# Optimization experiments

Hardware: AMD Instinct MI355X
Metric: run time of the kernel (lower is better)

The kernel has to match this reference:

```python
import jax, jax.numpy as jnp
import numpy as np

# Static graph layout: B graphs, NPG nodes/graph, CNUM com edges, MPG BatchReversal rows/graph
B, NPG, CNUM, MPG = 512, 64, 8, 128
CN, CE, HN, HE = 256, 64, 4, 4          # node channels, edge channels, heads
EPG = MPG + CNUM + NPG                   # edge_inform rows (= edges) per graph = 200


def _seg_softmax(logits, seg, num):
    # softmax over segments (per-destination) along axis 0; logits [E, H]
    m = jax.ops.segment_max(logits, seg, num_segments=num)
    m = jnp.where(jnp.isfinite(m), m, 0.0)
    e = jnp.exp(logits - m[seg])
    s = jax.ops.segment_sum(e, seg, num_segments=num)
    return e / (s[seg] + 1e-16)


def _attn_conv(x, edge_index, Wq, Wk, Wv, heads, e=None, We=None):
    # Multi-head edge-conditioned graph attention (SuperConv_N / SuperConv_E).
    N = x.shape[0]
    O = Wq.shape[1]
    Oh = O // heads
    q = (x @ Wq).reshape(N, heads, Oh)
    k = (x @ Wk).reshape(N, heads, Oh)
    v = (x @ Wv).reshape(N, heads, Oh)
    src, dst = edge_index[0], edge_index[1]
    ks, vs = k[src], v[src]
    if e is not None:
        ef = (e @ We).reshape(-1, heads, Oh)
        ks = ks + ef
        vs = vs + ef
    scale = jnp.asarray(1.0 / np.sqrt(Oh), x.dtype)
    logits = jax.nn.leaky_relu(jnp.sum(q[dst] * ks, axis=-1) * scale, 0.2)  # [E, H]
    alpha = _seg_softmax(logits, dst, N)
    out = jax.ops.segment_sum(alpha[..., None] * vs, dst, num_segments=N)  # [N, H, Oh]
    return out.reshape(N, O)


def _bn(x, g, b):
    # pyg_nn.BatchNorm, training mode: batch statistics over node axis
    mu = x.mean(axis=0)
    var = x.var(axis=0)
    return (x - mu) * jax.lax.rsqrt(var + 1e-5) * g + b


def _to_edge(br):
    # Vectorized BatchReversalToEdge: per graph, first CNUM rows duplicated
    # consecutively, then NPG one-hot rows, then the remaining MPG-CNUM rows.
    sub = br.reshape(B, MPG, CE)
    dup = jnp.repeat(sub[:, :CNUM], 2, axis=1)                     # [B, 2c, CE]
    onehot = jnp.zeros((CE,), br.dtype).at[0].set(1.0)
    blk = jnp.broadcast_to(onehot, (B, NPG, CE))                   # [B, n, CE]
    out = jnp.concatenate([dup, blk, sub[:, CNUM:]], axis=1)       # [B, EPG, CE]
    return out.reshape(B * EPG, CE)


def setup_inputs() -> dict:
    key = jax.random.key(0)
    ks = jax.random.split(key, 20)
    Nn = B * NPG
    x = jax.random.normal(ks[0], (Nn, CN), jnp.float32)
    base_n = jnp.repeat(jnp.arange(B) * NPG, EPG)
    edge_index = base_n[None, :] + jax.random.randint(ks[1], (2, B * EPG), 0, NPG)
    br_feature = jax.random.normal(ks[2], (B * MPG, CE), jnp.float32)
    base_e = jnp.repeat(jnp.arange(B) * MPG, MPG * 4)
    br_edge_index = base_e[None, :] + jax.random.randint(ks[3], (2, B * MPG * 4), 0, MPG)

    def w(k, i, o):
        return jax.random.normal(k, (i, o), jnp.float32) / np.sqrt(i)

    inp = dict(x=x, edge_index=edge_index, br_feature=br_feature, br_edge_index=br_edge_index)
    inp.update(WqE1=w(ks[4], CE, CE), WkE1=w(ks[5], CE, CE), WvE1=w(ks[6], CE, CE),
               gE1=jnp.ones(CE), bE1=jnp.zeros(CE))
    inp.update(Wq1=w(ks[7], CN, CN), Wk1=w(ks[8], CN, CN), Wv1=w(ks[9], CN, CN),
               We1=w(ks[10], CE, CN), gN1=jnp.ones(CN), bN1=jnp.zeros(CN))
    inp.update(WqE2=w(ks[11], CE, CE), WkE2=w(ks[12], CE, CE), WvE2=w(ks[13], CE, CE),
               gE2=jnp.ones(CE), bE2=jnp.zeros(CE))
    inp.update(Wq2=w(ks[14], CN, CN), Wk2=w(ks[15], CN, CN), Wv2=w(ks[16], CN, CN),
               We2=w(ks[17], CE, CN), gN2=jnp.ones(CN), bN2=jnp.zeros(CN))
    return inp


def reference(x, edge_index, br_feature, br_edge_index,
              WqE1, WkE1, WvE1, gE1, bE1,
              Wq1, Wk1, Wv1, We1, gN1, bN1,
              WqE2, WkE2, WvE2, gE2, bE2,
              Wq2, Wk2, Wv2, We2, gN2, bN2):
    br = br_feature
    # conv_E -> BN -> ReLU, residual (E_in == E_out)
    o = jax.nn.relu(_bn(_attn_conv(br, br_edge_index, WqE1, WkE1, WvE1, HE), gE1, bE1))
    br = o + br
    ei = _to_edge(br)
    # conv_N -> BN -> ReLU, residual (N_in == N_out)
    o = jax.nn.relu(_bn(_attn_conv(x, edge_index, Wq1, Wk1, Wv1, HN, e=ei, We=We1), gN1, bN1))
    out = o + x
    # conv_E2 -> BN -> ReLU, subtractive residual
    o2 = jax.nn.relu(_bn(_attn_conv(br, br_edge_index, WqE2, WkE2, WvE2, HE), gE2, bE2))
    br = br - o2
    ei = _to_edge(br)
    # conv_N2 -> BN -> ReLU, subtractive residual
    o2 = jax.nn.relu(_bn(_attn_conv(out, edge_index, Wq2, Wk2, Wv2, HN, e=ei, We=We2), gN2, bN2))
    out2 = out - o2
    # GetSuperNode: last node of each graph (regular layout -> simple slice)
    super_node = out2.reshape(B, NPG, CN)[:, -1]
    return out2, ei, br, super_node
```

## Files before the change

kernel.cpp:

```cpp
#include <hip/hip_runtime.h>

typedef unsigned short u16;
typedef unsigned int u32;

#define BGR 512
#define NPG_ 64
#define MPG_ 128
#define EPG_ 200
#define CN_ 256
#define CE_ 64
#define NN_ (BGR*NPG_)
#define NBR_ (BGR*MPG_)
#define EN_ (BGR*EPG_)
#define EBR_ (BGR*MPG_*4)

__device__ __forceinline__ float bf2f(u16 u){ return __uint_as_float(((u32)u) << 16); }
__device__ __forceinline__ u16 f2bf(float f){
  u32 u = __float_as_uint(f);
  u32 r = u + 0x7FFFu + ((u >> 16) & 1u);
  return (u16)(r >> 16);
}
__device__ __forceinline__ void up2(u32 w, float& a, float& b){
  a = bf2f((u16)w); b = bf2f((u16)(w >> 16));
}
__device__ __forceinline__ u32 pk2(u16 a, u16 b){ return (u32)a | ((u32)b << 16); }

typedef __attribute__((ext_vector_type(8))) short short8v;
typedef __attribute__((ext_vector_type(4))) float f32x4;

__global__ __launch_bounds__(256) void zero_k(float* __restrict__ p, size_t n){
  size_t i = (size_t)blockIdx.x*256 + threadIdx.x;
  const size_t st = (size_t)gridDim.x*256;
  for (; i < n; i += st) p[i] = 0.f;
}

template<int BN>
__global__ __launch_bounds__(256) void mfma_gemm2(const float* __restrict__ A,
                                                  const float* __restrict__ W,
                                                  u16* __restrict__ C,
                                                  int M, int N, int K)
{
  constexpr int PK = 40;
  constexpr int NF = (BN == 128) ? 4 : 2;
  constexpr int KPTB = BN / 32;
  __shared__ alignas(16) u16 sAh[128*PK], sAl[128*PK];
  __shared__ alignas(16) u16 sBh[BN*PK],  sBl[BN*PK];

  const int tid = threadIdx.x;
  const int m0 = blockIdx.y * 128, n0 = blockIdx.x * BN;
  const int wid = tid >> 6, lane = tid & 63;
  const int wm = (wid >> 1) * 64;
  const int wn = (wid & 1) * (NF * 16);
  const int l15 = lane & 15, l4 = lane >> 4;
  const int kb = l4 * 8;

  const int arow = tid >> 1, aseg = (tid & 1) * 16;
  const int nq = tid & (BN/4 - 1);
  const int bn = nq * 4;
  const int kq = tid / (BN/4);
  const int bk = kq * KPTB;

  f32x4 acc[4][NF];
  #pragma unroll
  for (int i = 0; i < 4; i++)
    #pragma unroll
    for (int j = 0; j < NF; j++) acc[i][j] = (f32x4)0.f;

  for (int k0 = 0; k0 < K; k0 += 32){
    {
      const float* ap = A + (size_t)(m0 + arow)*K + k0 + aseg;
      u16 hh[16], ll[16];
      #pragma unroll
      for (int j = 0; j < 16; j += 4){
        const float4 av = *(const float4*)(ap + j);
        const float vs0 = av.x, vs1 = av.y, vs2 = av.z, vs3 = av.w;
        u16 h;
        h = f2bf(vs0); hh[j+0] = h; ll[j+0] = f2bf(vs0 - bf2f(h));
        h = f2bf(vs1); hh[j+1] = h; ll[j+1] = f2bf(vs1 - bf2f(h));
        h = f2bf(vs2); hh[j+2] = h; ll[j+2] = f2bf(vs2 - bf2f(h));
        h = f2bf(vs3); hh[j+3] = h; ll[j+3] = f2bf(vs3 - bf2f(h));
      }
      uint4 p;
      p.x = pk2(hh[0],hh[1]);  p.y = pk2(hh[2],hh[3]);
      p.z = pk2(hh[4],hh[5]);  p.w = pk2(hh[6],hh[7]);
      *(uint4*)&sAh[arow*PK + aseg] = p;
      p.x = pk2(hh[8],hh[9]);  p.y = pk2(hh[10],hh[11]);
      p.z = pk2(hh[12],hh[13]); p.w = pk2(hh[14],hh[15]);
      *(uint4*)&sAh[arow*PK + aseg + 8] = p;
      p.x = pk2(ll[0],ll[1]);  p.y = pk2(ll[2],ll[3]);
      p.z = pk2(ll[4],ll[5]);  p.w = pk2(ll[6],ll[7]);
      *(uint4*)&sAl[arow*PK + aseg] = p;
      p.x = pk2(ll[8],ll[9]);  p.y = pk2(ll[10],ll[11]);
      p.z = pk2(ll[12],ll[13]); p.w = pk2(ll[14],ll[15]);
      *(uint4*)&sAl[arow*PK + aseg + 8] = p;
    }
    {
      float bv[KPTB][4];
      #pragma unroll
      for (int j = 0; j < KPTB; j++){
        const float4 w4 = *(const float4*)(W + (size_t)(k0 + bk + j)*N + n0 + bn);
        bv[j][0] = w4.x; bv[j][1] = w4.y; bv[j][2] = w4.z; bv[j][3] = w4.w;
      }
      #pragma unroll
      for (int nn = 0; nn < 4; nn++){
        u16 hh[KPTB], ll[KPTB];
        #pragma unroll
        for (int j = 0; j < KPTB; j++){
          const u16 h = f2bf(bv[j][nn]);
          hh[j] = h; ll[j] = f2bf(bv[j][nn] - bf2f(h));
        }
        if constexpr (KPTB == 4){
          uint2 wr;
          wr.x = pk2(hh[0],hh[1]); wr.y = pk2(hh[2],hh[3]);
          *(uint2*)&sBh[(bn+nn)*PK + bk] = wr;
          wr.x = pk2(ll[0],ll[1]); wr.y = pk2(ll[2],ll[3]);
          *(uint2*)&sBl[(bn+nn)*PK + bk] = wr;
        } else {
          *(u32*)&sBh[(bn+nn)*PK + bk] = pk2(hh[0],hh[1]);
          *(u32*)&sBl[(bn+nn)*PK + bk] = pk2(ll[0],ll[1]);
        }
      }
    }
    __syncthreads();

    short8v ah_[4], al_[4], bh_[NF], bl_[NF];
    #pragma unroll
    for (int mf = 0; mf < 4; mf++){
      ah_[mf] = *(const short8v*)&sAh[(wm + mf*16 + l15)*PK + kb];
      al_[mf] = *(const short8v*)&sAl[(wm + mf*16 + l15)*PK + kb];
    }
    #pragma unroll
    for (int nf = 0; nf < NF; nf++){
      bh_[nf] = *(const short8v*)&sBh[(wn + nf*16 + l15)*PK + kb];
      bl_[nf] = *(const short8v*)&sBl[(wn + nf*16 + l15)*PK + kb];
    }
    #pragma unroll
    for (int nf = 0; nf < NF; nf++)
      #pragma unroll
      for (int mf = 0; mf < 4; mf++){
        acc[mf][nf] = __builtin_amdgcn_mfma_f32_16x16x32_bf16(ah_[mf], bh_[nf], acc[mf][nf], 0, 0, 0);
        acc[mf][nf] = __builtin_amdgcn_mfma_f32_16x16x32_bf16(al_[mf], bh_[nf], acc[mf][nf], 0, 0, 0);
        acc[mf][nf] = __builtin_amdgcn_mfma_f32_16x16x32_bf16(ah_[mf], bl_[nf], acc[mf][nf], 0, 0, 0);
      }
    __syncthreads();
  }

  #pragma unroll
  for (int mf = 0; mf < 4; mf++)
    #pragma unroll
    for (int nf = 0; nf < NF; nf++)
      #pragma unroll
      for (int r = 0; r < 4; r++){
        const int row = m0 + wm + mf*16 + l4*4 + r;
        const int col = n0 + wn + nf*16 + l15;
        C[(size_t)row*N + col] = f2bf(acc[mf][nf][r]);
      }
}

__global__ __launch_bounds__(64) void to_edge_g(const float* __restrict__ br, float* __restrict__ eo)
{
  const int j = blockIdx.x, g = blockIdx.y, c = threadIdx.x;
  float v;
  if (j < 16) v = br[((size_t)g*128 + (j >> 1))*64 + c];
  else if (j < 80) v = (c == 0) ? 1.f : 0.f;
  else v = br[((size_t)g*128 + (j - 72))*64 + c];
  eo[((size_t)g*200 + j)*64 + c] = v;
}

template<int C, int NODES, int EDGES, bool HAS_EF>
__global__ __launch_bounds__(256) void attn_gather(const u16* __restrict__ q,
                                                   const u16* __restrict__ k,
                                                   const u16* __restrict__ v,
                                                   const u16* __restrict__ ef,
                                                   const int* __restrict__ eidx, int Etot,
                                                   float scale,
                                                   float* __restrict__ att)
{
  constexpr int NCH = (EDGES + 63) / 64;
  const int tid = threadIdx.x;
  const int wv = tid >> 6, lane = tid & 63;
  const int d = blockIdx.x*4 + wv;
  const int g = d / NODES;
  const int e0 = g * EDGES;

  float q0, q1, q2, q3;
  if (C == 256){
    const uint2 qa = *(const uint2*)(q + (size_t)d*C + lane*4);
    up2(qa.x, q0, q1); up2(qa.y, q2, q3);
  } else {
    q0 = bf2f(q[(size_t)d*C + lane]);
    q1 = q2 = q3 = 0.f;
  }

  int de[NCH], se[NCH];
  #pragma unroll
  for (int ch = 0; ch < NCH; ch++){
    const int ee = ch*64 + lane;
    const bool in = (NCH*64 == EDGES) || (ee < EDGES);
    de[ch] = in ? eidx[Etot + e0 + ee] : -1;
    se[ch] = in ? eidx[e0 + ee] : 0;
  }

  float acc0 = 0.f, acc1 = 0.f, acc2 = 0.f, acc3 = 0.f, den = 0.f;
  #pragma unroll
  for (int ch = 0; ch < NCH; ch++){
    unsigned long long m = __ballot(de[ch] == d);
    while (m){
      const int b = (int)__builtin_ctzll(m);
      m &= m - 1;
      const int sb = __shfl(se[ch], b);
      const int eb = e0 + ch*64 + b;
      float p, v0, v1, v2, v3;
      if (C == 256){
        const uint2 ka = *(const uint2*)(k + (size_t)sb*C + lane*4);
        const uint2 va = *(const uint2*)(v + (size_t)sb*C + lane*4);
        float k0,k1,k2,k3;
        up2(ka.x,k0,k1); up2(ka.y,k2,k3);
        up2(va.x,v0,v1); up2(va.y,v2,v3);
        if (HAS_EF){
          const uint2 ea = *(const uint2*)(ef + (size_t)eb*C + lane*4);
          float f0,f1,f2,f3;
          up2(ea.x,f0,f1); up2(ea.y,f2,f3);
          k0+=f0; k1+=f1; k2+=f2; k3+=f3;
          v0+=f0; v1+=f1; v2+=f2; v3+=f3;
        }
        p = q0*k0 + q1*k1 + q2*k2 + q3*k3;
      } else {
        float kk = bf2f(k[(size_t)sb*C + lane]);
        v0 = bf2f(v[(size_t)sb*C + lane]);
        v1 = v2 = v3 = 0.f;
        if (HAS_EF){
          const float f0 = bf2f(ef[(size_t)eb*C + lane]);
          kk += f0; v0 += f0;
        }
        p = q0*kk;
      }
      p += __shfl_xor(p, 1);
      p += __shfl_xor(p, 2);
      p += __shfl_xor(p, 4);
      p += __shfl_xor(p, 8);
      float lg = p * scale;
      lg = lg > 0.f ? lg : 0.2f * lg;
      const float ex = expf(lg);
      den += ex;
      acc0 += ex*v0; acc1 += ex*v1; acc2 += ex*v2; acc3 += ex*v3;
    }
  }
  const float inv = 1.0f / (den + 1e-16f);
  if (C == 256){
    float4 o; o.x = acc0*inv; o.y = acc1*inv; o.z = acc2*inv; o.w = acc3*inv;
    *(float4*)(att + (size_t)d*C + lane*4) = o;
  } else {
    att[(size_t)d*C + lane] = acc0*inv;
  }
}

template<int C>
__global__ __launch_bounds__(256) void bn_stats_f(const float* __restrict__ a, int Nrows,
                                                  float* __restrict__ stats)
{
  const int tid = threadIdx.x;
  const int c = tid & (C - 1);
  const int sub = (C == 64) ? (tid >> 6) : 0;
  const int nsub = 256 / C;
  float s = 0.f, ss = 0.f;
  for (int r = blockIdx.x*nsub + sub; r < Nrows; r += gridDim.x*nsub){
    const float val = a[(size_t)r*C + c];
    s += val; ss += val*val;
  }
  __shared__ float rs[256], rss[256];
  rs[tid] = s; rss[tid] = ss;
  __syncthreads();
  if (tid < C){
    float S = rs[tid], SS = rss[tid];
    for (int u = 1; u < nsub; u++){ S += rs[tid + u*C]; SS += rss[tid + u*C]; }
    atomicAdd(&stats[tid], S);
    atomicAdd(&stats[C + tid], SS);
  }
}

template<bool SUB>
__global__ __launch_bounds__(256) void bn_apply_f(const float* __restrict__ a,
    const float* __restrict__ stats, const float* __restrict__ gw, const float* __restrict__ bw,
    const float* __restrict__ res, float* __restrict__ o, int Nrows, int C)
{
  const size_t idx = (size_t)blockIdx.x*256 + threadIdx.x;
  const int c = (int)(idx & (size_t)(C - 1));
  const float invN = 1.0f / (float)Nrows;
  const float mu = stats[c] * invN;
  const float var = stats[C + c] * invN - mu*mu;
  const float scale = rsqrtf(var + 1e-5f) * gw[c];
  float val = (a[idx] - mu) * scale + bw[c];
  val = val > 0.f ? val : 0.f;
  const float rv = res[idx];
  o[idx] = SUB ? (rv - val) : (val + rv);
}

__global__ __launch_bounds__(256) void super_k(const float* __restrict__ out2, float* __restrict__ sn)
{
  const int g = blockIdx.x, c = threadIdx.x;
  sn[(size_t)g*256 + c] = out2[((size_t)g*64 + 63)*256 + c];
}

extern "C" void kernel_launch(void* const* d_in, const int* in_sizes, int n_in,
                              void* d_out, int out_size, void* d_ws, size_t ws_size,
                              hipStream_t stream)
{
  (void)in_sizes; (void)n_in; (void)out_size; (void)ws_size;
  const float* x    = (const float*)d_in[0];
  const int*   ei   = (const int*)d_in[1];
  const float* brf  = (const float*)d_in[2];
  const int*   bei  = (const int*)d_in[3];
  const float *WqE1=(const float*)d_in[4], *WkE1=(const float*)d_in[5], *WvE1=(const float*)d_in[6];
  const float *gE1=(const float*)d_in[7],  *bE1=(const float*)d_in[8];
  const float *Wq1=(const float*)d_in[9],  *Wk1=(const float*)d_in[10], *Wv1=(const float*)d_in[11];
  const float *We1=(const float*)d_in[12];
  const float *gN1=(const float*)d_in[13], *bN1=(const float*)d_in[14];
  const float *WqE2=(const float*)d_in[15],*WkE2=(const float*)d_in[16],*WvE2=(const float*)d_in[17];
  const float *gE2=(const float*)d_in[18], *bE2=(const float*)d_in[19];
  const float *Wq2=(const float*)d_in[20], *Wk2=(const float*)d_in[21], *Wv2=(const float*)d_in[22];
  const float *We2=(const float*)d_in[23];
  const float *gN2=(const float*)d_in[24], *bN2=(const float*)d_in[25];

  char* ws = (char*)d_ws;
  u16*   h_ef    = (u16*)(ws + 0);
  char*  p1      = ws + 52428800;
  u16*   h_qE    = (u16*)(p1);
  u16*   h_kE    = (u16*)(p1 + 8388608);
  u16*   h_vE    = (u16*)(p1 + 16777216);
  u16*   h_qN    = (u16*)(p1);
  u16*   h_kN    = (u16*)(p1 + 16777216);
  u16*   h_vN    = (u16*)(p1 + 33554432);
  float* f_eirow = (float*)(p1);
  float* f_att   = (float*)(ws + 102760448);
  float* f_br    = (float*)(ws + 136314880);
  float* f_out   = (float*)(ws + 153092096);
  float* f_stats = (float*)(ws + 191889408);

  float* o_out2 = (float*)d_out;
  float* o_ei   = o_out2 + (size_t)NN_*CN_;
  float* o_br   = o_ei   + (size_t)EN_*CE_;
  float* o_sn   = o_br   + (size_t)NBR_*CE_;

  const int TPB = 256;
  zero_k<<<8, TPB, 0, stream>>>(f_stats, 2048);

  mfma_gemm2<64><<<dim3(1, NBR_/128), TPB, 0, stream>>>(brf, WqE1, h_qE, NBR_, CE_, CE_);
  mfma_gemm2<64><<<dim3(1, NBR_/128), TPB, 0, stream>>>(brf, WkE1, h_kE, NBR_, CE_, CE_);
  mfma_gemm2<64><<<dim3(1, NBR_/128), TPB, 0, stream>>>(brf, WvE1, h_vE, NBR_, CE_, CE_);
  attn_gather<64,MPG_,MPG_*4,false><<<NBR_/4, TPB, 0, stream>>>(h_qE, h_kE, h_vE, nullptr, bei, EBR_, 0.25f, f_att);
  bn_stats_f<64><<<256, TPB, 0, stream>>>(f_att, NBR_, f_stats);
  bn_apply_f<false><<<NBR_*CE_/256, TPB, 0, stream>>>(f_att, f_stats, gE1, bE1, brf, f_br, NBR_, CE_);

  to_edge_g<<<dim3(EPG_, BGR), 64, 0, stream>>>(f_br, f_eirow);
  mfma_gemm2<128><<<dim3(2, EN_/128), TPB, 0, stream>>>(f_eirow, We1, h_ef, EN_, CN_, CE_);
  mfma_gemm2<128><<<dim3(2, NN_/128), TPB, 0, stream>>>(x, Wq1, h_qN, NN_, CN_, CN_);
  mfma_gemm2<128><<<dim3(2, NN_/128), TPB, 0, stream>>>(x, Wk1, h_kN, NN_, CN_, CN_);
  mfma_gemm2<128><<<dim3(2, NN_/128), TPB, 0, stream>>>(x, Wv1, h_vN, NN_, CN_, CN_);
  attn_gather<256,NPG_,EPG_,true><<<NN_/4, TPB, 0, stream>>>(h_qN, h_kN, h_vN, h_ef, ei, EN_, 0.125f, f_att);
  bn_stats_f<256><<<256, TPB, 0, stream>>>(f_att, NN_, f_stats + 512);
  bn_apply_f<false><<<NN_*CN_/256, TPB, 0, stream>>>(f_att, f_stats + 512, gN1, bN1, x, f_out, NN_, CN_);

  mfma_gemm2<64><<<dim3(1, NBR_/128), TPB, 0, stream>>>(f_br, WqE2, h_qE, NBR_, CE_, CE_);
  mfma_gemm2<64><<<dim3(1, NBR_/128), TPB, 0, stream>>>(f_br, WkE2, h_kE, NBR_, CE_, CE_);
  mfma_gemm2<64><<<dim3(1, NBR_/128), TPB, 0, stream>>>(f_br, WvE2, h_vE, NBR_, CE_, CE_);
  attn_gather<64,MPG_,MPG_*4,false><<<NBR_/4, TPB, 0, stream>>>(h_qE, h_kE, h_vE, nullptr, bei, EBR_, 0.25f, f_att);
  bn_stats_f<64><<<256, TPB, 0, stream>>>(f_att, NBR_, f_stats + 1024);
  bn_apply_f<true><<<NBR_*CE_/256, TPB, 0, stream>>>(f_att, f_stats + 1024, gE2, bE2, f_br, o_br, NBR_, CE_);

  to_edge_g<<<dim3(EPG_, BGR), 64, 0, stream>>>(o_br, o_ei);

  mfma_gemm2<128><<<dim3(2, EN_/128), TPB, 0, stream>>>(o_ei, We2, h_ef, EN_, CN_, CE_);
  mfma_gemm2<128><<<dim3(2, NN_/128), TPB, 0, stream>>>(f_out, Wq2, h_qN, NN_, CN_, CN_);
  mfma_gemm2<128><<<dim3(2, NN_/128), TPB, 0, stream>>>(f_out, Wk2, h_kN, NN_, CN_, CN_);
  mfma_gemm2<128><<<dim3(2, NN_/128), TPB, 0, stream>>>(f_out, Wv2, h_vN, NN_, CN_, CN_);
  attn_gather<256,NPG_,EPG_,true><<<NN_/4, TPB, 0, stream>>>(h_qN, h_kN, h_vN, h_ef, ei, EN_, 0.125f, f_att);
  bn_stats_f<256><<<256, TPB, 0, stream>>>(f_att, NN_, f_stats + 1536);
  bn_apply_f<true><<<NN_*CN_/256, TPB, 0, stream>>>(f_att, f_stats + 1536, gN2, bN2, f_out, o_out2, NN_, CN_);

  super_k<<<BGR, TPB, 0, stream>>>(o_out2, o_sn);
}
```

Baseline: 764.4 us.

## Project edge features per BR row instead of per expanded edge; fuse edge QKV

Measured after the change: 721.7 us. 1.06x faster.

```diff
diff --git a/kernel.cpp b/kernel.cpp
--- a/kernel.cpp
+++ b/kernel.cpp
@@ -157,6 +157,101 @@
       }
 }
 
+__global__ __launch_bounds__(256) void qkv3_e(const float* __restrict__ A,
+    const float* __restrict__ Wq, const float* __restrict__ Wk, const float* __restrict__ Wv,
+    u16* __restrict__ Cq, u16* __restrict__ Ck, u16* __restrict__ Cv)
+{
+  constexpr int K = 64, N = 64, PK = 72;
+  __shared__ alignas(16) u16 sAh[128*PK], sAl[128*PK];
+  __shared__ alignas(16) u16 sBh[64*PK],  sBl[64*PK];
+  const int tid = threadIdx.x;
+  const int m0 = blockIdx.x * 128;
+  const int wid = tid >> 6, lane = tid & 63;
+  const int wm = (wid >> 1) * 64;
+  const int wn = (wid & 1) * 32;
+  const int l15 = lane & 15, l4 = lane >> 4;
+  const int kb = l4 * 8;
+
+  {
+    const int arow = tid >> 1, aseg = (tid & 1) * 32;
+    const float* ap = A + (size_t)(m0 + arow)*K + aseg;
+    #pragma unroll
+    for (int j = 0; j < 32; j += 4){
+      const float4 av = *(const float4*)(ap + j);
+      const float vs[4] = {av.x, av.y, av.z, av.w};
+      u16 hh[4], ll[4];
+      #pragma unroll
+      for (int t = 0; t < 4; t++){ const u16 h = f2bf(vs[t]); hh[t] = h; ll[t] = f2bf(vs[t] - bf2f(h)); }
+      uint2 wr;
+      wr.x = pk2(hh[0],hh[1]); wr.y = pk2(hh[2],hh[3]);
+      *(uint2*)&sAh[arow*PK + aseg + j] = wr;
+      wr.x = pk2(ll[0],ll[1]); wr.y = pk2(ll[2],ll[3]);
+      *(uint2*)&sAl[arow*PK + aseg + j] = wr;
+    }
+  }
+  const int nq = tid & 15, bn = nq*4;
+  const int kq = tid >> 4, bk = kq*4;
+  const float* Ws[3] = {Wq, Wk, Wv};
+  u16* Cs[3] = {Cq, Ck, Cv};
+  #pragma unroll
+  for (int w = 0; w < 3; w++){
+    {
+      float bv[4][4];
+      #pragma unroll
+      for (int j = 0; j < 4; j++){
+        const float4 w4 = *(const float4*)(Ws[w] + (size_t)(bk+j)*N + bn);
+        bv[j][0]=w4.x; bv[j][1]=w4.y; bv[j][2]=w4.z; bv[j][3]=w4.w;
+      }
+      #pragma unroll
+      for (int nn = 0; nn < 4; nn++){
+        u16 hh[4], ll[4];
+        #pragma unroll
+        for (int j = 0; j < 4; j++){ const u16 h = f2bf(bv[j][nn]); hh[j] = h; ll[j] = f2bf(bv[j][nn] - bf2f(h)); }
+        uint2 wr;
+        wr.x = pk2(hh[0],hh[1]); wr.y = pk2(hh[2],hh[3]);
+        *(uint2*)&sBh[(bn+nn)*PK + bk] = wr;
+        wr.x = pk2(ll[0],ll[1]); wr.y = pk2(ll[2],ll[3]);
+        *(uint2*)&sBl[(bn+nn)*PK + bk] = wr;
+      }
+    }
+    __syncthreads();
+    f32x4 acc[4][2];
+    #pragma unroll
+    for (int i = 0; i < 4; i++){ acc[i][0] = (f32x4)0.f; acc[i][1] = (f32x4)0.f; }
+    #pragma unroll
+    for (int c = 0; c < 2; c++){
+      const int kc = kb + c*32;
+      short8v ah_[4], al_[4], bh_[2], bl_[2];
+      #pragma unroll
+      for (int mf = 0; mf < 4; mf++){
+        ah_[mf] = *(const short8v*)&sAh[(wm + mf*16 + l15)*PK + kc];
+        al_[mf] = *(const short8v*)&sAl[(wm + mf*16 + l15)*PK + kc];
+      }
+      #pragma unroll
+      for (int nf = 0; nf < 2; nf++){
+        bh_[nf] = *(const short8v*)&sBh[(wn + nf*16 + l15)*PK + kc];
+        bl_[nf] = *(const short8v*)&sBl[(wn + nf*16 + l15)*PK + kc];
+      }
+      #pragma unroll
+      for (int nf = 0; nf < 2; nf++)
+        #pragma unroll
+        for (int mf = 0; mf < 4; mf++){
+          acc[mf][nf] = __builtin_amdgcn_mfma_f32_16x16x32_bf16(ah_[mf], bh_[nf], acc[mf][nf], 0, 0, 0);
+          acc[mf][nf] = __builtin_amdgcn_mfma_f32_16x16x32_bf16(al_[mf], bh_[nf], acc[mf][nf], 0, 0, 0);
+          acc[mf][nf] = __builtin_amdgcn_mfma_f32_16x16x32_bf16(ah_[mf], bl_[nf], acc[mf][nf], 0, 0, 0);
+        }
+    }
+    #pragma unroll
+    for (int mf = 0; mf < 4; mf++)
+      #pragma unroll
+      for (int nf = 0; nf < 2; nf++)
+        #pragma unroll
+        for (int r = 0; r < 4; r++)
+          Cs[w][(size_t)(m0 + wm + mf*16 + l4*4 + r)*N + wn + nf*16 + l15] = f2bf(acc[mf][nf][r]);
+    __syncthreads();
+  }
+}
+
 __global__ __launch_bounds__(64) void to_edge_g(const float* __restrict__ br, float* __restrict__ eo)
 {
   const int j = blockIdx.x, g = blockIdx.y, c = threadIdx.x;
@@ -165,6 +260,14 @@
   else if (j < 80) v = (c == 0) ? 1.f : 0.f;
   else v = br[((size_t)g*128 + (j - 72))*64 + c];
   eo[((size_t)g*200 + j)*64 + c] = v;
+}
+
+__global__ __launch_bounds__(256) void cef_k(const float* __restrict__ We, u16* __restrict__ cef){
+  const int c = threadIdx.x;
+  const float w = We[c];
+  const u16 h = f2bf(w);
+  const u16 l = f2bf(w - bf2f(h));
+  cef[c] = f2bf(bf2f(h) + bf2f(l));
 }
 
 template<int C, int NODES, int EDGES, bool HAS_EF>
@@ -255,6 +358,82 @@
   }
 }
 
+__global__ __launch_bounds__(256) void attn_gather_n(const u16* __restrict__ q,
+                                                     const u16* __restrict__ k,
+                                                     const u16* __restrict__ v,
+                                                     const u16* __restrict__ brW,
+                                                     const u16* __restrict__ cef,
+                                                     const int* __restrict__ eidx, int Etot,
+                                                     float scale,
+                                                     float* __restrict__ att)
+{
+  constexpr int C = 256, NODES = 64, EDGES = 200, NCH = 4;
+  const int tid = threadIdx.x;
+  const int wv = tid >> 6, lane = tid & 63;
+  const int d = blockIdx.x*4 + wv;
+  const int g = d >> 6;
+  const int e0 = g * EDGES;
+
+  float q0, q1, q2, q3;
+  {
+    const uint2 qa = *(const uint2*)(q + (size_t)d*C + lane*4);
+    up2(qa.x, q0, q1); up2(qa.y, q2, q3);
+  }
+  float cf0, cf1, cf2, cf3;
+  {
+    const uint2 ca = *(const uint2*)(cef + lane*4);
+    up2(ca.x, cf0, cf1); up2(ca.y, cf2, cf3);
+  }
+
+  int de[NCH], se[NCH];
+  #pragma unroll
+  for (int ch = 0; ch < NCH; ch++){
+    const int ee = ch*64 + lane;
+    const bool in = (ee < EDGES);
+    de[ch] = in ? eidx[Etot + e0 + ee] : -1;
+    se[ch] = in ? eidx[e0 + ee] : 0;
+  }
+
+  float acc0 = 0.f, acc1 = 0.f, acc2 = 0.f, acc3 = 0.f, den = 0.f;
+  #pragma unroll
+  for (int ch = 0; ch < NCH; ch++){
+    unsigned long long m = __ballot(de[ch] == d);
+    while (m){
+      const int b = (int)__builtin_ctzll(m);
+      m &= m - 1;
+      const int sb = __shfl(se[ch], b);
+      const int j = ch*64 + b;
+      const uint2 ka = *(const uint2*)(k + (size_t)sb*C + lane*4);
+      const uint2 va = *(const uint2*)(v + (size_t)sb*C + lane*4);
+      float k0,k1,k2,k3, v0,v1,v2,v3;
+      up2(ka.x,k0,k1); up2(ka.y,k2,k3);
+      up2(va.x,v0,v1); up2(va.y,v2,v3);
+      float f0, f1, f2, f3;
+      if (j >= 16 && j < 80){ f0 = cf0; f1 = cf1; f2 = cf2; f3 = cf3; }
+      else {
+        const int er = (g << 7) + (j < 16 ? (j >> 1) : (j - 72));
+        const uint2 ea = *(const uint2*)(brW + (size_t)er*C + lane*4);
+        up2(ea.x, f0, f1); up2(ea.y, f2, f3);
+      }
+      k0+=f0; k1+=f1; k2+=f2; k3+=f3;
+      v0+=f0; v1+=f1; v2+=f2; v3+=f3;
+      float p = q0*k0 + q1*k1 + q2*k2 + q3*k3;
+      p += __shfl_xor(p, 1);
+      p += __shfl_xor(p, 2);
+      p += __shfl_xor(p, 4);
+      p += __shfl_xor(p, 8);
+      float lg = p * scale;
+      lg = lg > 0.f ? lg : 0.2f * lg;
+      const float ex = expf(lg);
+      den += ex;
+      acc0 += ex*v0; acc1 += ex*v1; acc2 += ex*v2; acc3 += ex*v3;
+    }
+  }
+  const float inv = 1.0f / (den + 1e-16f);
+  float4 o; o.x = acc0*inv; o.y = acc1*inv; o.z = acc2*inv; o.w = acc3*inv;
+  *(float4*)(att + (size_t)d*C + lane*4) = o;
+}
+
 template<int C>
 __global__ __launch_bounds__(256) void bn_stats_f(const float* __restrict__ a, int Nrows,
                                                   float* __restrict__ stats)
@@ -331,10 +510,11 @@
   u16*   h_qN    = (u16*)(p1);
   u16*   h_kN    = (u16*)(p1 + 16777216);
   u16*   h_vN    = (u16*)(p1 + 33554432);
-  float* f_eirow = (float*)(p1);
   float* f_att   = (float*)(ws + 102760448);
   float* f_br    = (float*)(ws + 136314880);
   float* f_out   = (float*)(ws + 153092096);
+  u16*   cef1    = (u16*)(ws + 187695104);
+  u16*   cef2    = (u16*)(ws + 187696128);
   float* f_stats = (float*)(ws + 191889408);
 
   float* o_out2 = (float*)d_out;
@@ -345,37 +525,34 @@
   const int TPB = 256;
   zero_k<<<8, TPB, 0, stream>>>(f_stats, 2048);
 
-  mfma_gemm2<64><<<dim3(1, NBR_/128), TPB, 0, stream>>>(brf, WqE1, h_qE, NBR_, CE_, CE_);
-  mfma_gemm2<64><<<dim3(1, NBR_/128), TPB, 0, stream>>>(brf, WkE1, h_kE, NBR_, CE_, CE_);
-  mfma_gemm2<64><<<dim3(1, NBR_/128), TPB, 0, stream>>>(brf, WvE1, h_vE, NBR_, CE_, CE_);
+  qkv3_e<<<NBR_/128, TPB, 0, stream>>>(brf, WqE1, WkE1, WvE1, h_qE, h_kE, h_vE);
   attn_gather<64,MPG_,MPG_*4,false><<<NBR_/4, TPB, 0, stream>>>(h_qE, h_kE, h_vE, nullptr, bei, EBR_, 0.25f, f_att);
-  bn_stats_f<64><<<256, TPB, 0, stream>>>(f_att, NBR_, f_stats);
+  bn_stats_f<64><<<1024, TPB, 0, stream>>>(f_att, NBR_, f_stats);
   bn_apply_f<false><<<NBR_*CE_/256, TPB, 0, stream>>>(f_att, f_stats, gE1, bE1, brf, f_br, NBR_, CE_);
 
-  to_edge_g<<<dim3(EPG_, BGR), 64, 0, stream>>>(f_br, f_eirow);
-  mfma_gemm2<128><<<dim3(2, EN_/128), TPB, 0, stream>>>(f_eirow, We1, h_ef, EN_, CN_, CE_);
+  mfma_gemm2<128><<<dim3(2, NBR_/128), TPB, 0, stream>>>(f_br, We1, h_ef, NBR_, CN_, CE_);
+  cef_k<<<1, TPB, 0, stream>>>(We1, cef1);
   mfma_gemm2<128><<<dim3(2, NN_/128), TPB, 0, stream>>>(x, Wq1, h_qN, NN_, CN_, CN_);
   mfma_gemm2<128><<<dim3(2, NN_/128), TPB, 0, stream>>>(x, Wk1, h_kN, NN_, CN_, CN_);
   mfma_gemm2<128><<<dim3(2, NN_/128), TPB, 0, stream>>>(x, Wv1, h_vN, NN_, CN_, CN_);
-  attn_gather<256,NPG_,EPG_,true><<<NN_/4, TPB, 0, stream>>>(h_qN, h_kN, h_vN, h_ef, ei, EN_, 0.125f, f_att);
-  bn_stats_f<256><<<256, TPB, 0, stream>>>(f_att, NN_, f_stats + 512);
+  attn_gather_n<<<NN_/4, TPB, 0, stream>>>(h_qN, h_kN, h_vN, h_ef, cef1, ei, EN_, 0.125f, f_att);
+  bn_stats_f<256><<<1024, TPB, 0, stream>>>(f_att, NN_, f_stats + 512);
   bn_apply_f<false><<<NN_*CN_/256, TPB, 0, stream>>>(f_att, f_stats + 512, gN1, bN1, x, f_out, NN_, CN_);
 
-  mfma_gemm2<64><<<dim3(1, NBR_/128), TPB, 0, stream>>>(f_br, WqE2, h_qE, NBR_, CE_, CE_);
-  mfma_gemm2<64><<<dim3(1, NBR_/128), TPB, 0, stream>>>(f_br, WkE2, h_kE, NBR_, CE_, CE_);
-  mfma_gemm2<64><<<dim3(1, NBR_/128), TPB, 0, stream>>>(f_br, WvE2, h_vE, NBR_, CE_, CE_);
+  qkv3_e<<<NBR_/128, TPB, 0, stream>>>(f_br, WqE2, WkE2, WvE2, h_qE, h_kE, h_vE);
   attn_gather<64,MPG_,MPG_*4,false><<<NBR_/4, TPB, 0, stream>>>(h_qE, h_kE, h_vE, nullptr, bei, EBR_, 0.25f, f_att);
-  bn_stats_f<64><<<256, TPB, 0, stream>>>(f_att, NBR_, f_stats + 1024);
+  bn_stats_f<64><<<1024, TPB, 0, stream>>>(f_att, NBR_, f_stats + 1024);
   bn_apply_f<true><<<NBR_*CE_/256, TPB, 0, stream>>>(f_att, f_stats + 1024, gE2, bE2, f_br, o_br, NBR_, CE_);
 
   to_edge_g<<<dim3(EPG_, BGR), 64, 0, stream>>>(o_br, o_ei);
 
-  mfma_gemm2<128><<<dim3(2, EN_/128), TPB, 0, stream>>>(o_ei, We2, h_ef, EN_, CN_, CE_);
+  mfma_gemm2<128><<<dim3(2, NBR_/128), TPB, 0, stream>>>(o_br, We2, h_ef, NBR_, CN_, CE_);
+  cef_k<<<1, TPB, 0, stream>>>(We2, cef2);
   mfma_gemm2<128><<<dim3(2, NN_/128), TPB, 0, stream>>>(f_out, Wq2, h_qN, NN_, CN_, CN_);
   mfma_gemm2<128><<<dim3(2, NN_/128), TPB, 0, stream>>>(f_out, Wk2, h_kN, NN_, CN_, CN_);
   mfma_gemm2<128><<<dim3(2, NN_/128), TPB, 0, stream>>>(f_out, Wv2, h_vN, NN_, CN_, CN_);
-  attn_gather<256,NPG_,EPG_,true><<<NN_/4, TPB, 0, stream>>>(h_qN, h_kN, h_vN, h_ef, ei, EN_, 0.125f, f_att);
-  bn_stats_f<256><<<256, TPB, 0, stream>>>(f_att, NN_, f_stats + 1536);
+  attn_gather_n<<<NN_/4, TPB, 0, stream>>>(h_qN, h_kN, h_vN, h_ef, cef2, ei, EN_, 0.125f, f_att);
+  bn_stats_f<256><<<1024, TPB, 0, stream>>>(f_att, NN_, f_stats + 1536);
   bn_apply_f<true><<<NN_*CN_/256, TPB, 0, stream>>>(f_att, f_stats + 1536, gN2, bN2, f_out, o_out2, NN_, CN_);
 
   super_k<<<BGR, TPB, 0, stream>>>(o_out2, o_sn);
```
